# Optimization experiments

Measured on AMD Instinct MI355X. Metric: run time of the kernel, lower is better.

The kernel has to match this reference:

```python
import jax, jax.numpy as jnp
import numpy as np

B, S, E, P, H, F = 4, 4096, 256, 32, 8, 1024
DH = E // H
LN_EPS = 1e-5


def setup_inputs() -> dict:
    key = jax.random.key(0)
    ks = jax.random.split(key, 12)
    dt = jnp.float32
    return {
        "src": jax.random.normal(ks[0], (B, S, E), dt),
        "pos_embed": jax.random.normal(ks[1], (B, P, S), dt),
        # learnable positional transform (pos_linear: P -> P)
        "Wpos": jax.random.normal(ks[2], (P, P), dt) * (1.0 / np.sqrt(P)),
        "bpos": jnp.zeros((P,), dt),
        # RBF kernel hyperparameters (ScaleKernel(RBFKernel)) -- positive scalars
        "lengthscale": jnp.full((), 2.0, dt),
        "outputscale": jnp.full((), 1.0, dt),
        # value / output projections of multihead attention
        "Wv": jax.random.normal(ks[3], (E, E), dt) * (1.0 / np.sqrt(E)),
        "bv": jnp.zeros((E,), dt),
        "Wo": jax.random.normal(ks[4], (E, E), dt) * (1.0 / np.sqrt(E)),
        "bo": jnp.zeros((E,), dt),
        # feed-forward
        "W1": jax.random.normal(ks[5], (F, E), dt) * (1.0 / np.sqrt(E)),
        "b1": jnp.zeros((F,), dt),
        "W2": jax.random.normal(ks[6], (E, F), dt) * (1.0 / np.sqrt(F)),
        "b2": jnp.zeros((E,), dt),
        # layer norms
        "ln1_g": jnp.ones((E,), dt), "ln1_b": jnp.zeros((E,), dt),
        "ln2_g": jnp.ones((E,), dt), "ln2_b": jnp.zeros((E,), dt),
    }


def _layer_norm(x, g, b):
    mu = jnp.mean(x, -1, keepdims=True)
    var = jnp.mean(jnp.square(x - mu), -1, keepdims=True)
    return (x - mu) * jax.lax.rsqrt(var + LN_EPS) * g + b


def _rbf_scores(x, lengthscale, outputscale):
    # x: [B, S, P] -> scaled RBF kernel matrix [B, S, S]
    xs = x / lengthscale
    sq = jnp.sum(xs * xs, axis=-1)  # [B, S]
    d2 = sq[:, :, None] + sq[:, None, :] - 2.0 * jnp.einsum('bsp,btp->bst', xs, xs)
    d2 = jnp.maximum(d2, 0.0)
    return outputscale * jnp.exp(-0.5 * d2)


def reference(src, pos_embed, Wpos, bpos, lengthscale, outputscale,
              Wv, bv, Wo, bo, W1, b1, W2, b2, ln1_g, ln1_b, ln2_g, ln2_b):
    b, s, e = src.shape
    # learnable positional transform: [B,P,S] -> [B,S,P] -> linear -> back
    pe = jnp.einsum('bps,op->bos', pos_embed, Wpos) + bpos[None, :, None]  # [B,P,S]
    # GP-kernel attention scores over sequence positions
    scores = _rbf_scores(pe.transpose(0, 2, 1), lengthscale, outputscale)  # [B,S,S]
    attn = jax.nn.softmax(scores, axis=-1)
    # value projection, per-head weighted sum (scores shared across heads)
    v = (src @ Wv.T + bv).reshape(b, s, H, DH)
    ctx = jnp.einsum('bqk,bkhd->bqhd', attn, v).reshape(b, s, e)
    attn_out = ctx @ Wo.T + bo
    x = _layer_norm(src + attn_out, ln1_g, ln1_b)
    ff = jax.nn.relu(x @ W1.T + b1) @ W2.T + b2
    return _layer_norm(x + ff, ln2_g, ln2_b)
```

## Files before the change

### kernel.cpp

```cpp
#include <hip/hip_runtime.h>
#include <stdint.h>

#define BN 4
#define SN 4096
#define EN 256
#define PN 32
#define FN 1024
#define BS (BN*SN)
#define PAUG 64

typedef uint16_t bf16_t;
typedef short v4s  __attribute__((ext_vector_type(4)));
typedef short v8s  __attribute__((ext_vector_type(8)));
typedef __bf16 bf16x8 __attribute__((ext_vector_type(8)));
typedef float v4f   __attribute__((ext_vector_type(4)));
typedef float v16f  __attribute__((ext_vector_type(16)));

#define MFMA16(a,b,c) __builtin_amdgcn_mfma_f32_16x16x32_bf16(a,b,c,0,0,0)
#define MFMA32(a,b,c) __builtin_amdgcn_mfma_f32_32x32x16_bf16(a,b,c,0,0,0)

__device__ __forceinline__ float b2f(bf16_t x){
    uint32_t u = ((uint32_t)x) << 16; float f; __builtin_memcpy(&f, &u, 4); return f;
}
__device__ __forceinline__ bf16_t f2b(float f){
    uint32_t u; __builtin_memcpy(&u, &f, 4);
    u += 0x7FFFu + ((u >> 16) & 1u);
    return (bf16_t)(u >> 16);
}
__device__ __forceinline__ bf16x8 ldb8(const bf16_t* p){
    v8s r = *(const v8s*)p; return __builtin_bit_cast(bf16x8, r);
}
__device__ __forceinline__ bf16x8 ldb8u(const bf16_t* p){
    v4s lo = *(const v4s*)p;
    v4s hi = *(const v4s*)(p + 4);
    v8s r = __builtin_shufflevector(lo, hi, 0,1,2,3,4,5,6,7);
    return __builtin_bit_cast(bf16x8, r);
}
__device__ __forceinline__ float ldsc(const float* p){ return *p; }
__device__ __forceinline__ float ldsc(const bf16_t* p){ return b2f(*p); }
__device__ __forceinline__ void stsc(float* p, float v){ *p = v; }
__device__ __forceinline__ void stsc(bf16_t* p, float v){ *p = f2b(v); }

#if __has_builtin(__builtin_amdgcn_cvt_pk_bf16_f32)
typedef __bf16 bf16x2 __attribute__((ext_vector_type(2)));
__device__ __forceinline__ uint32_t pkbf16(float a, float b){
    bf16x2 r = __builtin_amdgcn_cvt_pk_bf16_f32(a, b);
    return __builtin_bit_cast(uint32_t, r);
}
#else
__device__ __forceinline__ uint32_t pkbf16(float a, float b){
    return (uint32_t)f2b(a) | ((uint32_t)f2b(b) << 16);
}
#endif

typedef const __attribute__((address_space(1))) uint32_t* glds_gp;
typedef __attribute__((address_space(3))) uint32_t* glds_lp;
__device__ __forceinline__ void glds16(const bf16_t* g, bf16_t* l){
    __builtin_amdgcn_global_load_lds((glds_gp)g, (glds_lp)l, 16, 0, 0);
}

__global__ __launch_bounds__(256) void prep_kernel(
    const float* __restrict__ src, bf16_t* __restrict__ srcb,
    const float* __restrict__ Wv, bf16_t* __restrict__ Wvb,
    const float* __restrict__ Wo, bf16_t* __restrict__ Wob,
    const float* __restrict__ W1, bf16_t* __restrict__ W1b,
    const float* __restrict__ W2, bf16_t* __restrict__ W2b,
    const float* __restrict__ pos, const float* __restrict__ Wp,
    const float* __restrict__ bp,  const float* __restrict__ lsp,
    bf16_t* __restrict__ xk, bf16_t* __restrict__ xq)
{
    __shared__ float Wsh[PN*PN];
    __shared__ float bsh[PN];
    int bid = blockIdx.x;
    int tid = threadIdx.x;

    if (bid < 4736){
        const float* sp; bf16_t* dp; int off;
        if (bid < 4096){ sp = src; dp = srcb; off = (bid*256 + tid)*4; }
        else {
            int i = ((bid - 4096)*256 + tid)*4;
            if      (i <  65536){ sp=Wv; dp=Wvb; off=i; }
            else if (i < 131072){ sp=Wo; dp=Wob; off=i- 65536; }
            else if (i < 393216){ sp=W1; dp=W1b; off=i-131072; }
            else                { sp=W2; dp=W2b; off=i-393216; }
        }
        float4 f = *(const float4*)(sp + off);
        v4s o;
        o.x = (short)f2b(f.x); o.y = (short)f2b(f.y);
        o.z = (short)f2b(f.z); o.w = (short)f2b(f.w);
        *(v4s*)(dp + off) = o;
        return;
    }

    int pb = bid - 4736;
    int b  = pb >> 4;
    int s  = (pb & 15)*256 + tid;

    for (int i = tid; i < PN*PN; i += 256) Wsh[i] = Wp[i];
    if (tid < PN) bsh[tid] = bp[tid];
    __syncthreads();

    float inv_ls = 1.0f / lsp[0];
    const float c1f = 1.4426950408889634f;

    float col[PN];
    #pragma unroll
    for (int p = 0; p < PN; p++) col[p] = pos[((size_t)b*PN + p)*SN + s];

    uint16_t xb[PN], qb[PN];
    float sq = 0.f;
    #pragma unroll 4
    for (int o = 0; o < PN; o++){
        float pe = bsh[o];
        #pragma unroll
        for (int p = 0; p < PN; p++) pe += col[p] * Wsh[o*PN + p];
        float pv = pe * inv_ls;
        uint16_t h = f2b(pv);
        xb[o] = h;
        qb[o] = f2b(c1f * pv);
        float xr = b2f(h);
        sq += xr * xr;
    }

    size_t base = ((size_t)b*SN + s) * PAUG;
    v8s pk[8];
    #pragma unroll
    for (int c = 0; c < 4; c++)
        #pragma unroll
        for (int j = 0; j < 8; j++) ((short*)&pk[c])[j] = (short)xb[c*8 + j];
    #pragma unroll
    for (int c = 4; c < 8; c++)
        #pragma unroll
        for (int j = 0; j < 8; j++) ((short*)&pk[c])[j] = 0;
    ((short*)&pk[4])[0] = (short)f2b(-0.5f * sq);
    ((short*)&pk[4])[1] = (short)0x3F80;
    #pragma unroll
    for (int c = 0; c < 8; c++) *(v8s*)(xk + base + c*8) = pk[c];

    #pragma unroll
    for (int c = 0; c < 4; c++)
        #pragma unroll
        for (int j = 0; j < 8; j++) ((short*)&pk[c])[j] = (short)qb[c*8 + j];
    ((short*)&pk[4])[0] = (short)f2b(c1f);
    ((short*)&pk[4])[1] = (short)f2b(-0.5f * sq * c1f);
    #pragma unroll
    for (int c = 0; c < 8; c++) *(v8s*)(xq + base + c*8) = pk[c];
}

template<int EPI, typename OutT>
__global__ __launch_bounds__(256) void gemm_t(
    const bf16_t* __restrict__ A, const bf16_t* __restrict__ W,
    const float* __restrict__ bias, OutT* __restrict__ out,
    bf16_t* __restrict__ vt, int N, int K)
{
    __shared__ __align__(16) bf16_t At[2][4096];
    __shared__ __align__(16) bf16_t Wt[2][4096];
    int tid = threadIdx.x;
    int lane = tid & 63, wv = tid >> 6, col = lane & 15, quad = lane >> 4;
    int m0 = blockIdx.x * 64, n0 = blockIdx.y * 64;
    int nck = K >> 6;

    int srow = tid >> 3;
    int spc  = (tid & 7) ^ (srow & 7);
    const bf16_t* asrc = A + (size_t)(m0 + srow)*K + spc*8;
    const bf16_t* wsrc = W + (size_t)(n0 + srow)*K + spc*8;

    v4f acc[4];
    #pragma unroll
    for (int t = 0; t < 4; t++) acc[t] = (v4f){0.f,0.f,0.f,0.f};

    glds16(asrc, &At[0][tid*8]);
    glds16(asrc + (size_t)32*K, &At[0][2048 + tid*8]);
    glds16(wsrc, &Wt[0][tid*8]);
    glds16(wsrc + (size_t)32*K, &Wt[0][2048 + tid*8]);
    __syncthreads();

    for (int c = 0; c < nck; c++){
        int cb = c & 1;
        if (c + 1 < nck){
            glds16(asrc + (c+1)*64, &At[cb^1][tid*8]);
            glds16(asrc + (size_t)32*K + (c+1)*64, &At[cb^1][2048 + tid*8]);
            glds16(wsrc + (c+1)*64, &Wt[cb^1][tid*8]);
            glds16(wsrc + (size_t)32*K + (c+1)*64, &Wt[cb^1][2048 + tid*8]);
        }
        #pragma unroll
        for (int kc = 0; kc < 2; kc++){
            int pc = ((kc*4 + quad) ^ (col & 7)) * 8;
            bf16x8 a = ldb8(&At[cb][(wv*16 + col)*64 + pc]);
            #pragma unroll
            for (int t = 0; t < 4; t++){
                bf16x8 b = ldb8(&Wt[cb][(t*16 + col)*64 + pc]);
                acc[t] = MFMA16(a, b, acc[t]);
            }
        }
        __syncthreads();
    }

    float bfv[4];
    #pragma unroll
    for (int t = 0; t < 4; t++) bfv[t] = bias[n0 + t*16 + col];

    if constexpr (EPI == 3){
        __shared__ uint16_t Tsh[64*74];
        #pragma unroll
        for (int r = 0; r < 4; r++)
            #pragma unroll
            for (int t = 0; t < 4; t++)
                Tsh[(wv*16 + quad*4 + r)*74 + t*16 + col] = f2b(acc[t][r] + bfv[t]);
        __syncthreads();
        int e = tid >> 2, sc = tid & 3;
        int b = m0 >> 12;
        int sl = (m0 & (SN-1)) + sc*16;
        v8s p0, p1;
        #pragma unroll
        for (int i = 0; i < 8; i++) ((short*)&p0)[i] = (short)Tsh[(sc*16 + i)*74 + e];
        #pragma unroll
        for (int i = 0; i < 8; i++) ((short*)&p1)[i] = (short)Tsh[(sc*16 + 8 + i)*74 + e];
        bf16_t* dst = vt + ((size_t)b*EN + n0 + e)*SN + sl;
        *(v8s*)dst = p0;
        *(v8s*)(dst + 8) = p1;
    } else {
        #pragma unroll
        for (int r = 0; r < 4; r++){
            int row = m0 + wv*16 + quad*4 + r;
            #pragma unroll
            for (int t = 0; t < 4; t++){
                float y = acc[t][r] + bfv[t];
                if constexpr (EPI == 1) y = fmaxf(y, 0.f);
                stsc(out + (size_t)row*N + n0 + t*16 + col, y);
            }
        }
    }
}

template<typename OutT, typename ResT>
__global__ __launch_bounds__(256) void ln_kernel(
    const bf16_t* __restrict__ y, const ResT* __restrict__ res,
    const float* __restrict__ gamma, const float* __restrict__ beta,
    OutT* __restrict__ out)
{
    int tid = threadIdx.x;
    int row = blockIdx.x * 32 + (tid >> 3);
    int l8  = tid & 7;
    size_t base = (size_t)row * EN;
    float v[32];
    float s1 = 0.f, s2 = 0.f;
    #pragma unroll
    for (int i = 0; i < 4; i++){
        int off = l8*8 + i*64;
        v8s a = *(const v8s*)(y + base + off);
        #pragma unroll
        for (int j = 0; j < 8; j++){
            float t = b2f((bf16_t)(uint16_t)a[j]) + ldsc(res + base + off + j);
            v[i*8 + j] = t; s1 += t; s2 += t*t;
        }
    }
    #pragma unroll
    for (int m = 1; m <= 4; m <<= 1){
        s1 += __shfl_xor(s1, m);
        s2 += __shfl_xor(s2, m);
    }
    float mu = s1 * (1.f/256.f);
    float rs = rsqrtf(s2 * (1.f/256.f) - mu*mu + 1e-5f);
    #pragma unroll
    for (int i = 0; i < 4; i++){
        int off = l8*8 + i*64;
        #pragma unroll
        for (int j = 0; j < 8; j++)
            stsc(out + base + off + j, (v[i*8+j]-mu)*rs*gamma[off+j] + beta[off+j]);
    }
}

__global__ __launch_bounds__(512, 4) void attn_kernel(
    const bf16_t* __restrict__ xk, const bf16_t* __restrict__ xq,
    const bf16_t* __restrict__ vt, const float* __restrict__ osp,
    bf16_t* __restrict__ ctx)
{
    __shared__ __align__(16) bf16_t Vl[256*128];
    __shared__ __align__(16) bf16_t Wtb[32*132];
    __shared__ float densh[8][32];
    __shared__ float dent[32];

    int tid  = threadIdx.x;
    int lane = tid & 63;
    int wv   = tid >> 6;
    int col  = lane & 15;
    int quad = lane >> 4;
    int l31  = lane & 31;
    int half = lane >> 5;

    int bid = blockIdx.x;
    int b   = (bid & 7) >> 1;
    int qi  = ((bid >> 3) << 1) | (bid & 1);
    int q0  = qi * 32;

    float k2 = 1.4426950408889634f * osp[0];

    const bf16_t* xkb = xk + (size_t)b * SN * PAUG;
    const bf16_t* xqb = xq + (size_t)b * SN * PAUG;
    const bf16_t* vtb = vt + (size_t)b * EN * SN;

    bf16x8 qf[2][2];
    #pragma unroll
    for (int g2 = 0; g2 < 2; g2++)
        #pragma unroll
        for (int h = 0; h < 2; h++)
            qf[g2][h] = ldb8(xqb + (size_t)(q0 + g2*16 + col)*PAUG + h*32 + quad*8);

    int erow = tid >> 4;
    int psw  = (tid & 15) ^ (erow & 15);
    const bf16_t* vsrc = vtb + (size_t)erow * SN + psw*8;

    v16f acc;
    #pragma unroll
    for (int i = 0; i < 16; i++) acc[i] = 0.f;
    float den[2] = {0.f, 0.f};
    const v4f zero = (v4f){0.f,0.f,0.f,0.f};

    for (int c = 0; c < 32; c++){
        #pragma unroll
        for (int j = 0; j < 8; j++)
            glds16(vsrc + (size_t)j*32*SN + c*128, &Vl[j*4096 + tid*8]);
        {
            const bf16_t* krow = xkb + (size_t)(c*128 + wv*16 + col)*PAUG;
            bf16x8 kf0 = ldb8(krow + quad*8);
            bf16x8 kf1 = ldb8(krow + 32 + quad*8);
            #pragma unroll
            for (int g2 = 0; g2 < 2; g2++){
                v4f st = MFMA16(kf0, qf[g2][0], zero);
                st = MFMA16(kf1, qf[g2][1], st);
                #pragma unroll
                for (int rp = 0; rp < 2; rp++){
                    float w0 = exp2f(fmaf(k2, exp2f(st[rp*2+0]), -k2));
                    float w1 = exp2f(fmaf(k2, exp2f(st[rp*2+1]), -k2));
                    den[g2] += w0 + w1;
                    *(uint32_t*)&Wtb[(g2*16+col)*132 + wv*16 + quad*4 + rp*2] = pkbf16(w0, w1);
                }
            }
        }
        __syncthreads();

        bf16x8 af[8];
        #pragma unroll
        for (int subk = 0; subk < 8; subk++)
            af[subk] = ldb8u(&Wtb[l31*132 + subk*16 + half*8]);
        int sw = l31 & 15;
        const bf16_t* vrow = &Vl[(wv*32 + l31)*128];
        #pragma unroll
        for (int subk = 0; subk < 8; subk++){
            bf16x8 bf = ldb8(vrow + ((subk*2 + half) ^ sw)*8);
            acc = MFMA32(af[subk], bf, acc);
        }
        __syncthreads();
    }

    #pragma unroll
    for (int g2 = 0; g2 < 2; g2++){
        den[g2] += __shfl_xor(den[g2], 16);
        den[g2] += __shfl_xor(den[g2], 32);
    }
    if (lane < 16){
        densh[wv][lane]      = den[0];
        densh[wv][16 + lane] = den[1];
    }
    __syncthreads();
    if (tid < 32){
        float s = 0.f;
        #pragma unroll
        for (int w = 0; w < 8; w++) s += densh[w][tid];
        dent[tid] = 1.f / s;
    }
    __syncthreads();

    size_t obase = ((size_t)b*SN + q0) * EN + wv*32;
    #pragma unroll
    for (int rg = 0; rg < 16; rg++){
        int row = (rg & 3) + 8*(rg >> 2) + 4*half;
        float inv = dent[row];
        ctx[obase + (size_t)row*EN + l31] = f2b(acc[rg] * inv);
    }
}

extern "C" void kernel_launch(void* const* d_in, const int* in_sizes, int n_in,
                              void* d_out, int out_size, void* d_ws, size_t ws_size,
                              hipStream_t stream)
{
    (void)in_sizes; (void)n_in; (void)out_size; (void)ws_size;
    const float* src  = (const float*)d_in[0];
    const float* pos  = (const float*)d_in[1];
    const float* Wpos = (const float*)d_in[2];
    const float* bpos = (const float*)d_in[3];
    const float* ls   = (const float*)d_in[4];
    const float* os   = (const float*)d_in[5];
    const float* Wv   = (const float*)d_in[6];
    const float* bv   = (const float*)d_in[7];
    const float* Wo   = (const float*)d_in[8];
    const float* bo   = (const float*)d_in[9];
    const float* W1   = (const float*)d_in[10];
    const float* b1   = (const float*)d_in[11];
    const float* W2   = (const float*)d_in[12];
    const float* b2   = (const float*)d_in[13];
    const float* g1   = (const float*)d_in[14];
    const float* be1  = (const float*)d_in[15];
    const float* g2   = (const float*)d_in[16];
    const float* be2  = (const float*)d_in[17];

    char* w = (char*)d_ws;
    bf16_t* xkb  = (bf16_t*)(w);
    bf16_t* xqb  = (bf16_t*)(w + ( 2u<<20));
    bf16_t* Wvb  = (bf16_t*)(w + ( 4u<<20));
    bf16_t* Wob  = (bf16_t*)(w + ( 4u<<20) + (1u<<18));
    bf16_t* W1b  = (bf16_t*)(w + ( 5u<<20));
    bf16_t* W2b  = (bf16_t*)(w + ( 6u<<20));
    bf16_t* srcb = (bf16_t*)(w + ( 8u<<20));
    bf16_t* y2   = (bf16_t*)(w + ( 8u<<20));
    bf16_t* vtg  = (bf16_t*)(w + (16u<<20));
    bf16_t* y1   = (bf16_t*)(w + (16u<<20));
    bf16_t* ctx  = (bf16_t*)(w + (24u<<20));
    bf16_t* xws  = (bf16_t*)(w + (24u<<20));
    bf16_t* hws  = (bf16_t*)(w + (32u<<20));

    prep_kernel<<<dim3(4800), 256, 0, stream>>>(
        src, srcb, Wv, Wvb, Wo, Wob, W1, W1b, W2, W2b,
        pos, Wpos, bpos, ls, xkb, xqb);

    gemm_t<3, bf16_t><<<dim3(BS/64, EN/64), 256, 0, stream>>>(
        srcb, Wvb, bv, (bf16_t*)nullptr, vtg, EN, EN);
    attn_kernel<<<dim3(512), 512, 0, stream>>>(xkb, xqb, vtg, os, ctx);
    gemm_t<0, bf16_t><<<dim3(BS/64, EN/64), 256, 0, stream>>>(
        ctx, Wob, bo, y1, (bf16_t*)nullptr, EN, EN);
    ln_kernel<bf16_t, bf16_t><<<dim3(BS/32), 256, 0, stream>>>(y1, srcb, g1, be1, xws);
    gemm_t<1, bf16_t><<<dim3(BS/64, FN/64), 256, 0, stream>>>(
        xws, W1b, b1, hws, (bf16_t*)nullptr, FN, EN);
    gemm_t<0, bf16_t><<<dim3(BS/64, EN/64), 256, 0, stream>>>(
        hws, W2b, b2, y2, (bf16_t*)nullptr, EN, FN);
    ln_kernel<float, bf16_t><<<dim3(BS/32), 256, 0, stream>>>(y2, xws, g2, be2, (float*)d_out);
}
```

Before: 278.0 us.

## Store V in MFMA fragment layout and load directly into registers, double-buffer weights

The V-projection epilogue now writes V in a layout matching the 32x32 MFMA B-operand fragments, so the attention kernel reads each lane's V fragment straight from global memory into registers instead of staging 64KB of V through LDS per chunk. The weight tile in LDS is double-buffered, which removes the second barrier per iteration, and the next chunk's key fragments are prefetched. It also uses the hardware exp2 builtin instead of exp2f. The aim is to cut LDS traffic and footprint and sync overhead, at the cost of more register pressure and reliance on L2 for V reuse across blocks.

```diff
diff --git a/kernel.cpp b/kernel.cpp
--- a/kernel.cpp
+++ b/kernel.cpp
@@ -40,6 +40,12 @@
 __device__ __forceinline__ float ldsc(const bf16_t* p){ return b2f(*p); }
 __device__ __forceinline__ void stsc(float* p, float v){ *p = v; }
 __device__ __forceinline__ void stsc(bf16_t* p, float v){ *p = f2b(v); }
+
+#if __has_builtin(__builtin_amdgcn_exp2f)
+__device__ __forceinline__ float fexp2(float x){ return __builtin_amdgcn_exp2f(x); }
+#else
+__device__ __forceinline__ float fexp2(float x){ return exp2f(x); }
+#endif
 
 #if __has_builtin(__builtin_amdgcn_cvt_pk_bf16_f32)
 typedef __bf16 bf16x2 __attribute__((ext_vector_type(2)));
@@ -210,15 +216,18 @@
         __syncthreads();
         int e = tid >> 2, sc = tid & 3;
         int b = m0 >> 12;
-        int sl = (m0 & (SN-1)) + sc*16;
+        int sbat = m0 & (SN-1);
+        int eb   = (n0 + e) >> 5;
+        int l31e = (n0 + e) & 31;
+        int k16  = (sbat >> 4) + sc;
         v8s p0, p1;
         #pragma unroll
         for (int i = 0; i < 8; i++) ((short*)&p0)[i] = (short)Tsh[(sc*16 + i)*74 + e];
         #pragma unroll
         for (int i = 0; i < 8; i++) ((short*)&p1)[i] = (short)Tsh[(sc*16 + 8 + i)*74 + e];
-        bf16_t* dst = vt + ((size_t)b*EN + n0 + e)*SN + sl;
+        bf16_t* dst = vt + ((((size_t)b*8 + eb)*256 + k16)*64 + l31e)*8;
         *(v8s*)dst = p0;
-        *(v8s*)(dst + 8) = p1;
+        *(v8s*)(dst + 256) = p1;
     } else {
         #pragma unroll
         for (int r = 0; r < 4; r++){
@@ -273,11 +282,10 @@
 
 __global__ __launch_bounds__(512, 4) void attn_kernel(
     const bf16_t* __restrict__ xk, const bf16_t* __restrict__ xq,
-    const bf16_t* __restrict__ vt, const float* __restrict__ osp,
+    const bf16_t* __restrict__ vf, const float* __restrict__ osp,
     bf16_t* __restrict__ ctx)
 {
-    __shared__ __align__(16) bf16_t Vl[256*128];
-    __shared__ __align__(16) bf16_t Wtb[32*132];
+    __shared__ __align__(16) bf16_t Wtb[2][32*132];
     __shared__ float densh[8][32];
     __shared__ float dent[32];
 
@@ -298,7 +306,7 @@
 
     const bf16_t* xkb = xk + (size_t)b * SN * PAUG;
     const bf16_t* xqb = xq + (size_t)b * SN * PAUG;
-    const bf16_t* vtb = vt + (size_t)b * EN * SN;
+    const bf16_t* vfb = vf + (((size_t)b*8 + wv)*256)*512 + lane*8;
 
     bf16x8 qf[2][2];
     #pragma unroll
@@ -306,10 +314,6 @@
         #pragma unroll
         for (int h = 0; h < 2; h++)
             qf[g2][h] = ldb8(xqb + (size_t)(q0 + g2*16 + col)*PAUG + h*32 + quad*8);
-
-    int erow = tid >> 4;
-    int psw  = (tid & 15) ^ (erow & 15);
-    const bf16_t* vsrc = vtb + (size_t)erow * SN + psw*8;
 
     v16f acc;
     #pragma unroll
@@ -317,41 +321,47 @@
     float den[2] = {0.f, 0.f};
     const v4f zero = (v4f){0.f,0.f,0.f,0.f};
 
+    const bf16_t* krow0 = xkb + (size_t)(wv*16 + col)*PAUG + quad*8;
+    bf16x8 kf0 = ldb8(krow0);
+    bf16x8 kf1 = ldb8(krow0 + 32);
+
     for (int c = 0; c < 32; c++){
-        #pragma unroll
-        for (int j = 0; j < 8; j++)
-            glds16(vsrc + (size_t)j*32*SN + c*128, &Vl[j*4096 + tid*8]);
-        {
-            const bf16_t* krow = xkb + (size_t)(c*128 + wv*16 + col)*PAUG;
-            bf16x8 kf0 = ldb8(krow + quad*8);
-            bf16x8 kf1 = ldb8(krow + 32 + quad*8);
-            #pragma unroll
-            for (int g2 = 0; g2 < 2; g2++){
-                v4f st = MFMA16(kf0, qf[g2][0], zero);
-                st = MFMA16(kf1, qf[g2][1], st);
-                #pragma unroll
-                for (int rp = 0; rp < 2; rp++){
-                    float w0 = exp2f(fmaf(k2, exp2f(st[rp*2+0]), -k2));
-                    float w1 = exp2f(fmaf(k2, exp2f(st[rp*2+1]), -k2));
-                    den[g2] += w0 + w1;
-                    *(uint32_t*)&Wtb[(g2*16+col)*132 + wv*16 + quad*4 + rp*2] = pkbf16(w0, w1);
-                }
+        int cb = c & 1;
+        bf16x8 vr[8];
+        #pragma unroll
+        for (int subk = 0; subk < 8; subk++)
+            vr[subk] = ldb8(vfb + (size_t)(c*8 + subk)*512);
+
+        #pragma unroll
+        for (int g2 = 0; g2 < 2; g2++){
+            v4f st = MFMA16(kf0, qf[g2][0], zero);
+            st = MFMA16(kf1, qf[g2][1], st);
+            #pragma unroll
+            for (int rp = 0; rp < 2; rp++){
+                float w0 = fexp2(fmaf(k2, fexp2(st[rp*2+0]), -k2));
+                float w1 = fexp2(fmaf(k2, fexp2(st[rp*2+1]), -k2));
+                den[g2] += w0 + w1;
+                *(uint32_t*)&Wtb[cb][(g2*16+col)*132 + wv*16 + quad*4 + rp*2] = pkbf16(w0, w1);
             }
         }
         __syncthreads();
 
-        bf16x8 af[8];
-        #pragma unroll
-        for (int subk = 0; subk < 8; subk++)
-            af[subk] = ldb8u(&Wtb[l31*132 + subk*16 + half*8]);
-        int sw = l31 & 15;
-        const bf16_t* vrow = &Vl[(wv*32 + l31)*128];
-        #pragma unroll
-        for (int subk = 0; subk < 8; subk++){
-            bf16x8 bf = ldb8(vrow + ((subk*2 + half) ^ sw)*8);
-            acc = MFMA32(af[subk], bf, acc);
-        }
-        __syncthreads();
+        if (c + 1 < 32){
+            const bf16_t* krow = xkb + (size_t)((c+1)*128 + wv*16 + col)*PAUG + quad*8;
+            kf0 = ldb8(krow);
+            kf1 = ldb8(krow + 32);
+        }
+
+        #pragma unroll
+        for (int sk4 = 0; sk4 < 2; sk4++){
+            bf16x8 af[4];
+            #pragma unroll
+            for (int j = 0; j < 4; j++)
+                af[j] = ldb8u(&Wtb[cb][l31*132 + (sk4*4 + j)*16 + half*8]);
+            #pragma unroll
+            for (int j = 0; j < 4; j++)
+                acc = MFMA32(af[j], vr[sk4*4 + j], acc);
+        }
     }
 
     #pragma unroll
```

Measured after the change: 258.2 us. -7.1%, faster.
